# Kernel tuning notes

Measured on AMD Instinct MI355X. Metric: run time of the kernel, lower is better.

Reference implementation:

```python
import jax, jax.numpy as jnp
import numpy as np
from jax import lax

B, L, D = 4, 4096, 1024
EXP = 2
DI = D * EXP
K_PERC = 7
KS_DIFF = 3
DILATIONS = (1, 4, 16)


def _dwconv(h, w, dil):
    # h: [B, C, L] channels-first, w: [C, 1, k] depthwise kernel (groups=C)
    k = w.shape[-1]
    pad = dil * (k // 2)
    return lax.conv_general_dilated(
        h, w, window_strides=(1,), padding=[(pad, pad)],
        rhs_dilation=(dil,), dimension_numbers=("NCH", "OIH", "NCH"),
        feature_group_count=w.shape[0])


def _layernorm(x, g, b, eps=1e-5):
    m = jnp.mean(x, axis=-1, keepdims=True)
    v = jnp.mean(jnp.square(x - m), axis=-1, keepdims=True)
    return (x - m) * lax.rsqrt(v + eps) * g + b


def setup_inputs() -> dict:
    key = jax.random.key(0)
    ks = jax.random.split(key, 16)
    n = lambda k, shape, scale: (jax.random.normal(k, shape, dtype=jnp.float32) * scale)
    inp = {
        "x": n(ks[0], (B, L, D), 1.0),
        # PerceptionFilter: 3 depthwise convs k=7, pointwise 3D->D, LayerNorm
        "pf_w0": n(ks[1], (D, 1, K_PERC), 0.3),
        "pf_w1": n(ks[2], (D, 1, K_PERC), 0.3),
        "pf_w2": n(ks[3], (D, 1, K_PERC), 0.3),
        "pf_pw": n(ks[4], (D, 3 * D), 1.0 / np.sqrt(3 * D)),
        "ln_g": jnp.ones((D,), jnp.float32),
        "ln_b": jnp.zeros((D,), jnp.float32),
        # ReactionGate: wu/wg: 2D->DI, wd: DI->D, alpha
        "rg_wu": n(ks[5], (DI, 2 * D), 1.0 / np.sqrt(2 * D)),
        "rg_wg": n(ks[6], (DI, 2 * D), 1.0 / np.sqrt(2 * D)),
        "rg_wd": n(ks[7], (D, DI), 1.0 / np.sqrt(DI)),
        "rg_alpha": jnp.full((D,), 0.1, jnp.float32),
        # MultiRateDiffusion: 3 depthwise dilated convs k=3, selector D->3, strength
        "md_w0": n(ks[8], (D, 1, KS_DIFF), 0.3),
        "md_w1": n(ks[9], (D, 1, KS_DIFF), 0.3),
        "md_w2": n(ks[10], (D, 1, KS_DIFF), 0.3),
        "md_sel": n(ks[11], (len(DILATIONS), D), 1.0 / np.sqrt(D)),
        "md_strength": jnp.asarray(0.1, jnp.float32),
    }
    return inp


def reference(x, pf_w0, pf_w1, pf_w2, pf_pw, ln_g, ln_b,
              rg_wu, rg_wg, rg_wd, rg_alpha,
              md_w0, md_w1, md_w2, md_sel, md_strength):
    # --- PerceptionFilter ---
    h = jnp.swapaxes(x, 1, 2)  # [B, D, L]
    pcat = jnp.concatenate([_dwconv(h, w, 1) for w in (pf_w0, pf_w1, pf_w2)], axis=1)  # [B, 3D, L]
    p = jnp.einsum("bcl,dc->bld", pcat, pf_pw)  # pointwise 1x1 conv -> [B, L, D]
    p = _layernorm(p, ln_g, ln_b)
    # --- ReactionGate ---
    cat = jnp.concatenate([x, p], axis=-1)  # [B, L, 2D]
    u = cat @ rg_wu.T
    g = jax.nn.sigmoid(cat @ rg_wg.T)
    x2 = x + rg_alpha * ((g * jax.nn.silu(u)) @ rg_wd.T)
    # --- MultiRateDiffusion ---
    h2 = jnp.swapaxes(x2, 1, 2)  # [B, D, L]
    diffs = jnp.stack([_dwconv(h2, w, dil) for w, dil in
                       zip((md_w0, md_w1, md_w2), DILATIONS)], axis=-1)  # [B, D, L, R]
    wsel = jax.nn.softmax(x2 @ md_sel.T, axis=-1)[:, None]  # [B, 1, L, R]
    combined = jnp.swapaxes(jnp.sum(diffs * wsel, axis=-1), 1, 2)  # [B, L, D]
    return x2 + md_strength * (combined - x2)
```

## Files before the change

### kernel.cpp

```cpp
#include <hip/hip_runtime.h>

#define LL 4096
#define BL 16384

typedef __attribute__((ext_vector_type(4))) float f32x4;
typedef __attribute__((ext_vector_type(4))) int i32x4;
typedef __attribute__((ext_vector_type(4))) unsigned short u16x4;
typedef unsigned short ushort_t;
typedef unsigned int u32;

static __device__ __forceinline__ unsigned short f2bf(float f) {
    union { float f; unsigned int i; } v; v.f = f;
    unsigned int r = v.i + 0x7fffu + ((v.i >> 16) & 1u);
    return (unsigned short)(r >> 16);
}
static __device__ __forceinline__ float bf2f(unsigned short u) {
    union { unsigned int i; float f; } v; v.i = ((unsigned int)u) << 16; return v.f;
}
static __device__ __forceinline__ int qclamp(float x, float s) {
    return (int)rintf(fminf(fmaxf(x * s, -127.f), 127.f));
}
static __device__ __forceinline__ int q4(float a, float b, float c, float d, float s) {
    return (qclamp(a,s) & 255) | ((qclamp(b,s) & 255) << 8) |
           ((qclamp(c,s) & 255) << 16) | ((qclamp(d,s) & 255) << 24);
}

static __device__ __forceinline__ i32x4 mfma_i8(i32x4 a, i32x4 b, i32x4 c) {
    asm("v_mfma_i32_16x16x64_i8 %0, %1, %2, %0" : "+v"(c) : "v"(a), "v"(b));
    return c;
}

static __device__ __forceinline__ void gload16(const char* g, char* l) {
    __builtin_amdgcn_global_load_lds(
        (const __attribute__((address_space(1))) u32*)g,
        (__attribute__((address_space(3))) u32*)l, 16, 0, 0);
}

#define BAR()   asm volatile("s_barrier" ::: "memory")
#define VMW0()  asm volatile("s_waitcnt vmcnt(0)" ::: "memory")

__global__ __launch_bounds__(256) void cvt_all(
    const float* __restrict__ wu, const float* __restrict__ wg,
    const float* __restrict__ pw, const float* __restrict__ wd,
    char* __restrict__ wug8, char* __restrict__ wpw8, char* __restrict__ wd8,
    float sW, float sW1)
{
    int blk = blockIdx.x;
    if (blk < 4096) {
        int r = blk;
        int type = (r >> 4) & 1;
        int src = ((r >> 5) << 4) | (r & 15);
        const float* sp = (type ? wg : wu) + (size_t)src * 2048;
        char* d = wug8 + (size_t)r * 2048;
        int i = threadIdx.x;
        f32x4 v0 = ((const f32x4*)sp)[2 * i];
        f32x4 v1 = ((const f32x4*)sp)[2 * i + 1];
        ((int*)d)[2 * i]     = q4(v0[0], v0[1], v0[2], v0[3], sW);
        ((int*)d)[2 * i + 1] = q4(v1[0], v1[1], v1[2], v1[3], sW);
    } else if (blk < 4096 + 3072) {
        int i = (blk - 4096) * 256 + threadIdx.x;
        f32x4 v = ((const f32x4*)pw)[i];
        ((int*)wpw8)[i] = q4(v[0], v[1], v[2], v[3], sW1);
    } else {
        int i = (blk - 4096 - 3072) * 256 + threadIdx.x;
        f32x4 v = ((const f32x4*)wd)[i];
        ((int*)wd8)[i] = q4(v[0], v[1], v[2], v[3], sW);
    }
}

__global__ __launch_bounds__(256) void pf_conv(
    const float* __restrict__ x,
    const float* __restrict__ w0, const float* __restrict__ w1, const float* __restrict__ w2,
    char* __restrict__ pcat, char* __restrict__ cat, float sP, float sX)
{
    int bl = blockIdx.x;
    int b = bl >> 12;
    int l = bl & 4095;
    int c0 = threadIdx.x << 2;

    f32x4 v[7];
#pragma unroll
    for (int t = 0; t < 7; ++t) {
        int ls = l + t - 3;
        if (ls >= 0 && ls < LL)
            v[t] = *(const f32x4*)(x + (((size_t)b * LL + ls) << 10) + c0);
        else {
            f32x4 z = {0.f, 0.f, 0.f, 0.f};
            v[t] = z;
        }
    }
    *(int*)(cat + (((size_t)bl) << 11) + c0) = q4(v[3][0], v[3][1], v[3][2], v[3][3], sX);
    const float* ww[3] = { w0, w1, w2 };
#pragma unroll
    for (int j = 0; j < 3; ++j) {
        const float* w = ww[j];
        float a[4];
#pragma unroll
        for (int e = 0; e < 4; ++e) {
            int c = c0 + e;
            float s = 0.f;
#pragma unroll
            for (int t = 0; t < 7; ++t) s += v[t][e] * w[c * 7 + t];
            a[e] = s;
        }
        *(int*)(pcat + (size_t)bl * 3072 + j * 1024 + c0) = q4(a[0], a[1], a[2], a[3], sP);
    }
}

__global__ __launch_bounds__(256) void ln_kernel(
    const ushort_t* __restrict__ p, const float* __restrict__ g,
    const float* __restrict__ bta, char* __restrict__ cat, float sX)
{
    int bl = blockIdx.x;
    int tid = threadIdx.x;
    int c0 = tid << 2;
    u16x4 pv = *(const u16x4*)(p + (((size_t)bl) << 10) + c0);
    float v0 = bf2f(pv[0]), v1 = bf2f(pv[1]), v2 = bf2f(pv[2]), v3 = bf2f(pv[3]);
    float s  = v0 + v1 + v2 + v3;
    float sq = v0*v0 + v1*v1 + v2*v2 + v3*v3;
#pragma unroll
    for (int off = 32; off > 0; off >>= 1) {
        s  += __shfl_down(s, off);
        sq += __shfl_down(sq, off);
    }
    __shared__ float rs[4], rq[4];
    int w = tid >> 6;
    if ((tid & 63) == 0) { rs[w] = s; rq[w] = sq; }
    __syncthreads();
    float S = rs[0] + rs[1] + rs[2] + rs[3];
    float Q = rq[0] + rq[1] + rq[2] + rq[3];
    float m   = S * (1.f / 1024.f);
    float var = Q * (1.f / 1024.f) - m * m;
    float inv = rsqrtf(var + 1e-5f);
    f32x4 gv = *(const f32x4*)(g + c0);
    f32x4 bv = *(const f32x4*)(bta + c0);
    *(int*)(cat + (((size_t)bl) << 11) + 1024 + c0) =
        q4((v0-m)*inv*gv[0]+bv[0], (v1-m)*inv*gv[1]+bv[1],
           (v2-m)*inv*gv[2]+bv[2], (v3-m)*inv*gv[3]+bv[3], sX);
}

template<int MODE>
__global__ __launch_bounds__(512, 2) void gemm8i(
    const char* __restrict__ A, const char* __restrict__ Bm,
    ushort_t* __restrict__ C16, char* __restrict__ C8,
    const float* __restrict__ X, const float* __restrict__ alpha,
    int N, int K, int lgny, float invS, float sOut)
{
    __shared__ char smem[131072];
    const int tid = threadIdx.x;
    const int wid = tid >> 6, lane = tid & 63;
    const int fr = lane & 15, fq = lane >> 4;
    const int wm = (wid >> 2) * 128;
    const int wn = (wid & 3) * 64;

    const int nwg = gridDim.x * gridDim.y;
    const int orig = blockIdx.y * gridDim.x + blockIdx.x;
    const int q = nwg >> 3;
    const int tile = (orig & 7) * q + (orig >> 3);
    const int m0 = (tile >> lgny) * 256;
    const int n0 = (tile & ((1 << lgny) - 1)) * 256;

    const int srow = tid >> 3;
    const int gch = ((tid & 7) ^ (srow & 7)) * 16;

    const char* gp[8];
    int lpo[8];
#pragma unroll
    for (int op = 0; op < 2; ++op)
#pragma unroll
        for (int j = 0; j < 4; ++j) {
            int idx = op * 4 + j;
            const char* gs = op ? Bm : A;
            int rb = op ? n0 : m0;
            gp[idx] = gs + (size_t)(rb + j * 64 + srow) * K + gch;
            lpo[idx] = op * 32768 + (j * 64 + srow) * 128 + (tid & 7) * 16;
        }

    const int ach0 = ((fq) ^ (fr & 7)) * 16;
    const int ach1 = ((4 + fq) ^ (fr & 7)) * 16;
    const int arow = (wm + fr) * 128;
    const int brow = 32768 + (wn + fr) * 128;

    i32x4 acc[8][4] = {};
    const int NT = K >> 7;

#define STAGE_ALL(koff, d) do {                                             \
    _Pragma("unroll") for (int i_ = 0; i_ < 8; ++i_)                        \
        gload16(gp[i_] + (koff), smem + (d) * 65536 + lpo[i_]);             \
    } while (0)

    STAGE_ALL(0, 0);
    VMW0();
    BAR();

    for (int t = 0; t < NT; ++t) {
        const int c = t & 1;
        const bool st = (t + 1 < NT);
        const char* base = smem + c * 65536;

        if (st) STAGE_ALL((size_t)(t + 1) * 128, c ^ 1);

        i32x4 b0[4], b1[4], a0[4], a1[4];
#pragma unroll
        for (int n_ = 0; n_ < 4; ++n_) {
            b0[n_] = *(const i32x4*)(base + brow + n_ * 2048 + ach0);
            b1[n_] = *(const i32x4*)(base + brow + n_ * 2048 + ach1);
        }
#pragma unroll
        for (int i_ = 0; i_ < 4; ++i_) {
            a0[i_] = *(const i32x4*)(base + arow + i_ * 2048 + ach0);
            a1[i_] = *(const i32x4*)(base + arow + i_ * 2048 + ach1);
        }
        __builtin_amdgcn_s_setprio(1);
#pragma unroll
        for (int i_ = 0; i_ < 4; ++i_)
#pragma unroll
            for (int n_ = 0; n_ < 4; ++n_) {
                acc[i_][n_] = mfma_i8(a0[i_], b0[n_], acc[i_][n_]);
                acc[i_][n_] = mfma_i8(a1[i_], b1[n_], acc[i_][n_]);
            }
        __builtin_amdgcn_s_setprio(0);
#pragma unroll
        for (int i_ = 0; i_ < 4; ++i_) {
            a0[i_] = *(const i32x4*)(base + arow + (4 + i_) * 2048 + ach0);
            a1[i_] = *(const i32x4*)(base + arow + (4 + i_) * 2048 + ach1);
        }
        __builtin_amdgcn_s_setprio(1);
#pragma unroll
        for (int i_ = 0; i_ < 4; ++i_)
#pragma unroll
            for (int n_ = 0; n_ < 4; ++n_) {
                acc[4 + i_][n_] = mfma_i8(a0[i_], b0[n_], acc[4 + i_][n_]);
                acc[4 + i_][n_] = mfma_i8(a1[i_], b1[n_], acc[4 + i_][n_]);
            }
        __builtin_amdgcn_s_setprio(0);

        if (st) VMW0();
        BAR();
    }
#undef STAGE_ALL

    const int mbase = m0 + wm + fq * 4;
#pragma unroll
    for (int mi = 0; mi < 8; ++mi) {
        if (MODE == 1) {
#pragma unroll
            for (int pi = 0; pi < 2; ++pi)
#pragma unroll
                for (int r = 0; r < 4; ++r) {
                    float u = (float)acc[mi][2 * pi][r] * invS;
                    float g = (float)acc[mi][2 * pi + 1][r] * invS;
                    float sg = 1.f / (1.f + __expf(-g));
                    float sl = u / (1.f + __expf(-u));
                    int col = ((n0 + wn) >> 1) + pi * 16 + fr;
                    C8[(size_t)(mbase + mi * 16 + r) * (N >> 1) + col] =
                        (char)qclamp(sg * sl, sOut);
                }
        } else {
#pragma unroll
            for (int ni = 0; ni < 4; ++ni)
#pragma unroll
                for (int r = 0; r < 4; ++r) {
                    int row = mbase + mi * 16 + r;
                    int col = n0 + wn + ni * 16 + fr;
                    size_t idx = (size_t)row * N + col;
                    float vv = (float)acc[mi][ni][r] * invS;
                    if (MODE == 0) C16[idx] = f2bf(vv);
                    else           C16[idx] = f2bf(X[idx] + alpha[col] * vv);
                }
        }
    }
}

__global__ __launch_bounds__(256) void diffusion(
    const ushort_t* __restrict__ x2,
    const float* __restrict__ w0, const float* __restrict__ w1, const float* __restrict__ w2,
    const float* __restrict__ sel, const float* __restrict__ strength_p,
    float* __restrict__ out)
{
    int bl = blockIdx.x;
    int b = bl >> 12;
    int l = bl & 4095;
    int tid = threadIdx.x;
    int c0 = tid << 2;
    const ushort_t* base = x2 + (((size_t)b * LL) << 10);

    u16x4 xcv = *(const u16x4*)(x2 + (((size_t)bl) << 10) + c0);
    float xc0 = bf2f(xcv[0]), xc1 = bf2f(xcv[1]), xc2 = bf2f(xcv[2]), xc3 = bf2f(xcv[3]);
    f32x4 s0 = *(const f32x4*)(sel + c0);
    f32x4 s1 = *(const f32x4*)(sel + 1024 + c0);
    f32x4 s2 = *(const f32x4*)(sel + 2048 + c0);
    float t0 = xc0*s0[0] + xc1*s0[1] + xc2*s0[2] + xc3*s0[3];
    float t1 = xc0*s1[0] + xc1*s1[1] + xc2*s1[2] + xc3*s1[3];
    float t2 = xc0*s2[0] + xc1*s2[1] + xc2*s2[2] + xc3*s2[3];
#pragma unroll
    for (int off = 32; off > 0; off >>= 1) {
        t0 += __shfl_down(t0, off);
        t1 += __shfl_down(t1, off);
        t2 += __shfl_down(t2, off);
    }
    __shared__ float r0[4], r1[4], r2[4];
    int w = tid >> 6;
    if ((tid & 63) == 0) { r0[w] = t0; r1[w] = t1; r2[w] = t2; }
    __syncthreads();
    float L0 = r0[0] + r0[1] + r0[2] + r0[3];
    float L1 = r1[0] + r1[1] + r1[2] + r1[3];
    float L2 = r2[0] + r2[1] + r2[2] + r2[3];
    float mx = fmaxf(L0, fmaxf(L1, L2));
    float e0 = __expf(L0 - mx), e1 = __expf(L1 - mx), e2 = __expf(L2 - mx);
    float inv = 1.f / (e0 + e1 + e2);
    float ws0 = e0 * inv, ws1 = e1 * inv, ws2 = e2 * inv;
    float stg = *strength_p;

    float comb0 = 0.f, comb1 = 0.f, comb2 = 0.f, comb3 = 0.f;
    const float* wset[3] = { w0, w1, w2 };
    const int dils[3] = { 1, 4, 16 };
    const float wsel[3] = { ws0, ws1, ws2 };
#pragma unroll
    for (int r = 0; r < 3; ++r) {
        const float* wp = wset[r] + (size_t)c0 * 3;
        float wf[12];
        *(f32x4*)&wf[0] = *(const f32x4*)(wp + 0);
        *(f32x4*)&wf[4] = *(const f32x4*)(wp + 4);
        *(f32x4*)&wf[8] = *(const f32x4*)(wp + 8);
        int dil = dils[r];
        float d0 = 0.f, d1 = 0.f, d2 = 0.f, d3 = 0.f;
#pragma unroll
        for (int t = 0; t < 3; ++t) {
            int ls = l + (t - 1) * dil;
            float xv0 = 0.f, xv1 = 0.f, xv2 = 0.f, xv3 = 0.f;
            if (ls >= 0 && ls < LL) {
                u16x4 xv = *(const u16x4*)(base + (((size_t)ls) << 10) + c0);
                xv0 = bf2f(xv[0]); xv1 = bf2f(xv[1]); xv2 = bf2f(xv[2]); xv3 = bf2f(xv[3]);
            }
            d0 += xv0 * wf[0 * 3 + t];
            d1 += xv1 * wf[1 * 3 + t];
            d2 += xv2 * wf[2 * 3 + t];
            d3 += xv3 * wf[3 * 3 + t];
        }
        comb0 += wsel[r] * d0; comb1 += wsel[r] * d1;
        comb2 += wsel[r] * d2; comb3 += wsel[r] * d3;
    }
    f32x4 o = { xc0 + stg * (comb0 - xc0), xc1 + stg * (comb1 - xc1),
                xc2 + stg * (comb2 - xc2), xc3 + stg * (comb3 - xc3) };
    *(f32x4*)(out + (((size_t)bl) << 10) + c0) = o;
}

extern "C" void kernel_launch(void* const* d_in, const int* in_sizes, int n_in,
                              void* d_out, int out_size, void* d_ws, size_t ws_size,
                              hipStream_t stream)
{
    const float* x      = (const float*)d_in[0];
    const float* pf_w0  = (const float*)d_in[1];
    const float* pf_w1  = (const float*)d_in[2];
    const float* pf_w2  = (const float*)d_in[3];
    const float* pf_pw  = (const float*)d_in[4];
    const float* ln_g   = (const float*)d_in[5];
    const float* ln_b   = (const float*)d_in[6];
    const float* rg_wu  = (const float*)d_in[7];
    const float* rg_wg  = (const float*)d_in[8];
    const float* rg_wd  = (const float*)d_in[9];
    const float* rg_al  = (const float*)d_in[10];
    const float* md_w0  = (const float*)d_in[11];
    const float* md_w1  = (const float*)d_in[12];
    const float* md_w2  = (const float*)d_in[13];
    const float* md_sel = (const float*)d_in[14];
    const float* md_str = (const float*)d_in[15];
    float* outp = (float*)d_out;

    const float sP  = 127.f / 5.f;
    const float sX  = 127.f / 6.f;
    const float sW1 = 127.f / 0.11f;
    const float sW  = 127.f / 0.14f;
    const float invS1 = 1.f / (sP * sW1);
    const float invS2 = 1.f / (sX * sW);

    char* ws = (char*)d_ws;
    size_t off = 0;
    char*     pcat8 = (char*)   (ws + off); off += (size_t)BL * 3072;
    char*     cat8  = (char*)   (ws + off); off += (size_t)BL * 2048;
    ushort_t* ppre  = (ushort_t*)(ws + off); off += (size_t)BL * 1024 * 2;
    char*     wpw8  = (char*)   (ws + off); off += (size_t)1024 * 3072;
    char*     wug8  = (char*)   (ws + off); off += (size_t)4096 * 2048;
    char*     wd8   = (char*)   (ws + off); off += (size_t)1024 * 2048;
    char*     act8  = pcat8;
    ushort_t* x2    = ppre;

    cvt_all<<<4096 + 3072 + 2048, 256, 0, stream>>>(
        rg_wu, rg_wg, pf_pw, rg_wd, wug8, wpw8, wd8, sW, sW1);

    pf_conv<<<BL, 256, 0, stream>>>(x, pf_w0, pf_w1, pf_w2, pcat8, cat8, sP, sX);

    gemm8i<0><<<dim3(64, 4), 512, 0, stream>>>(
        pcat8, wpw8, ppre, nullptr, nullptr, nullptr, 1024, 3072, 2, invS1, 0.f);

    ln_kernel<<<BL, 256, 0, stream>>>(ppre, ln_g, ln_b, cat8, sX);

    gemm8i<1><<<dim3(64, 16), 512, 0, stream>>>(
        cat8, wug8, nullptr, act8, nullptr, nullptr, 4096, 2048, 4, invS2, sX);

    gemm8i<2><<<dim3(64, 4), 512, 0, stream>>>(
        act8, wd8, x2, nullptr, x, rg_al, 1024, 2048, 2, invS2, 0.f);

    diffusion<<<BL, 256, 0, stream>>>(x2, md_w0, md_w1, md_w2, md_sel, md_str, outp);
}
```

Baseline: 451.2 us.

## Switch int8 GEMM to 32x32x32 MFMA tiles with reworked fragment loads

Replaces the 16x16x64 int8 MFMA with the 32x32x32 variant, so each wave computes 4x2 blocks of 32x32 accumulators instead of 8x4 blocks of 16x16. LDS fragment addressing and swizzle are recomputed for the new lane mapping. The epilogues are rewritten, with the gated MODE 1 path using a lane shuffle to pair u and g columns. The aim is fewer LDS fragment reads per MFMA. The trade-off is a more complex epilogue, half-idle lanes in the gated store, and possible correctness risk in the interleaved u/g column mapping.

Result: slower. 537.2 us (+19.1%).

```diff
diff --git a/kernel.cpp b/kernel.cpp
--- a/kernel.cpp
+++ b/kernel.cpp
@@ -5,6 +5,7 @@
 
 typedef __attribute__((ext_vector_type(4))) float f32x4;
 typedef __attribute__((ext_vector_type(4))) int i32x4;
+typedef __attribute__((ext_vector_type(16))) int i32x16;
 typedef __attribute__((ext_vector_type(4))) unsigned short u16x4;
 typedef unsigned short ushort_t;
 typedef unsigned int u32;
@@ -25,8 +26,8 @@
            ((qclamp(c,s) & 255) << 16) | ((qclamp(d,s) & 255) << 24);
 }
 
-static __device__ __forceinline__ i32x4 mfma_i8(i32x4 a, i32x4 b, i32x4 c) {
-    asm("v_mfma_i32_16x16x64_i8 %0, %1, %2, %0" : "+v"(c) : "v"(a), "v"(b));
+static __device__ __forceinline__ i32x16 mfma_i8_32(i32x4 a, i32x4 b, i32x16 c) {
+    asm("v_mfma_i32_32x32x32_i8 %0, %1, %2, %0" : "+v"(c) : "v"(a), "v"(b));
     return c;
 }
 
@@ -149,7 +150,7 @@
     __shared__ char smem[131072];
     const int tid = threadIdx.x;
     const int wid = tid >> 6, lane = tid & 63;
-    const int fr = lane & 15, fq = lane >> 4;
+    const int l31 = lane & 31, hi = lane >> 5, l7 = lane & 7;
     const int wm = (wid >> 2) * 128;
     const int wn = (wid & 3) * 64;
 
@@ -176,12 +177,13 @@
             lpo[idx] = op * 32768 + (j * 64 + srow) * 128 + (tid & 7) * 16;
         }
 
-    const int ach0 = ((fq) ^ (fr & 7)) * 16;
-    const int ach1 = ((4 + fq) ^ (fr & 7)) * 16;
-    const int arow = (wm + fr) * 128;
-    const int brow = 32768 + (wn + fr) * 128;
-
-    i32x4 acc[8][4] = {};
+    int chk[4];
+#pragma unroll
+    for (int ks = 0; ks < 4; ++ks) chk[ks] = ((ks * 2 + hi) ^ l7) * 16;
+    const int arow = (wm + l31) * 128;
+    const int brow = 32768 + (wn + l31) * 128;
+
+    i32x16 acc[4][2] = {};
     const int NT = K >> 7;
 
 #define STAGE_ALL(koff, d) do {                                             \
@@ -200,76 +202,66 @@
 
         if (st) STAGE_ALL((size_t)(t + 1) * 128, c ^ 1);
 
-        i32x4 b0[4], b1[4], a0[4], a1[4];
-#pragma unroll
-        for (int n_ = 0; n_ < 4; ++n_) {
-            b0[n_] = *(const i32x4*)(base + brow + n_ * 2048 + ach0);
-            b1[n_] = *(const i32x4*)(base + brow + n_ * 2048 + ach1);
-        }
-#pragma unroll
-        for (int i_ = 0; i_ < 4; ++i_) {
-            a0[i_] = *(const i32x4*)(base + arow + i_ * 2048 + ach0);
-            a1[i_] = *(const i32x4*)(base + arow + i_ * 2048 + ach1);
-        }
-        __builtin_amdgcn_s_setprio(1);
-#pragma unroll
-        for (int i_ = 0; i_ < 4; ++i_)
-#pragma unroll
-            for (int n_ = 0; n_ < 4; ++n_) {
-                acc[i_][n_] = mfma_i8(a0[i_], b0[n_], acc[i_][n_]);
-                acc[i_][n_] = mfma_i8(a1[i_], b1[n_], acc[i_][n_]);
-            }
-        __builtin_amdgcn_s_setprio(0);
-#pragma unroll
-        for (int i_ = 0; i_ < 4; ++i_) {
-            a0[i_] = *(const i32x4*)(base + arow + (4 + i_) * 2048 + ach0);
-            a1[i_] = *(const i32x4*)(base + arow + (4 + i_) * 2048 + ach1);
-        }
-        __builtin_amdgcn_s_setprio(1);
-#pragma unroll
-        for (int i_ = 0; i_ < 4; ++i_)
-#pragma unroll
-            for (int n_ = 0; n_ < 4; ++n_) {
-                acc[4 + i_][n_] = mfma_i8(a0[i_], b0[n_], acc[4 + i_][n_]);
-                acc[4 + i_][n_] = mfma_i8(a1[i_], b1[n_], acc[4 + i_][n_]);
-            }
-        __builtin_amdgcn_s_setprio(0);
+#pragma unroll
+        for (int h = 0; h < 2; ++h) {
+            i32x4 b[2][2], a[4][2];
+#pragma unroll
+            for (int ti = 0; ti < 2; ++ti)
+#pragma unroll
+                for (int s_ = 0; s_ < 2; ++s_)
+                    b[ti][s_] = *(const i32x4*)(base + brow + ti * 4096 + chk[2 * h + s_]);
+#pragma unroll
+            for (int mi = 0; mi < 4; ++mi)
+#pragma unroll
+                for (int s_ = 0; s_ < 2; ++s_)
+                    a[mi][s_] = *(const i32x4*)(base + arow + mi * 4096 + chk[2 * h + s_]);
+            __builtin_amdgcn_s_setprio(1);
+#pragma unroll
+            for (int mi = 0; mi < 4; ++mi)
+#pragma unroll
+                for (int ti = 0; ti < 2; ++ti)
+#pragma unroll
+                    for (int s_ = 0; s_ < 2; ++s_)
+                        acc[mi][ti] = mfma_i8_32(a[mi][s_], b[ti][s_], acc[mi][ti]);
+            __builtin_amdgcn_s_setprio(0);
+        }
 
         if (st) VMW0();
         BAR();
     }
 #undef STAGE_ALL
 
-    const int mbase = m0 + wm + fq * 4;
-#pragma unroll
-    for (int mi = 0; mi < 8; ++mi) {
-        if (MODE == 1) {
-#pragma unroll
-            for (int pi = 0; pi < 2; ++pi)
-#pragma unroll
-                for (int r = 0; r < 4; ++r) {
-                    float u = (float)acc[mi][2 * pi][r] * invS;
-                    float g = (float)acc[mi][2 * pi + 1][r] * invS;
+#pragma unroll
+    for (int mi = 0; mi < 4; ++mi)
+#pragma unroll
+        for (int ti = 0; ti < 2; ++ti) {
+            if (MODE == 1) {
+                int colb = ((n0 + wn + ti * 32) >> 1) + (lane & 15);
+#pragma unroll
+                for (int r = 0; r < 16; ++r) {
+                    int val = acc[mi][ti][r];
+                    int pv = __shfl_xor(val, 16);
+                    float u = (float)((lane & 16) ? pv : val) * invS;
+                    float g = (float)((lane & 16) ? val : pv) * invS;
                     float sg = 1.f / (1.f + __expf(-g));
                     float sl = u / (1.f + __expf(-u));
-                    int col = ((n0 + wn) >> 1) + pi * 16 + fr;
-                    C8[(size_t)(mbase + mi * 16 + r) * (N >> 1) + col] =
-                        (char)qclamp(sg * sl, sOut);
+                    if (!(lane & 16)) {
+                        int row = m0 + wm + mi * 32 + (r & 3) + 8 * (r >> 2) + 4 * hi;
+                        C8[(size_t)row * (N >> 1) + colb] = (char)qclamp(sg * sl, sOut);
+                    }
                 }
-        } else {
-#pragma unroll
-            for (int ni = 0; ni < 4; ++ni)
-#pragma unroll
-                for (int r = 0; r < 4; ++r) {
-                    int row = mbase + mi * 16 + r;
-                    int col = n0 + wn + ni * 16 + fr;
+            } else {
+                int col = n0 + wn + ti * 32 + l31;
+#pragma unroll
+                for (int r = 0; r < 16; ++r) {
+                    int row = m0 + wm + mi * 32 + (r & 3) + 8 * (r >> 2) + 4 * hi;
                     size_t idx = (size_t)row * N + col;
-                    float vv = (float)acc[mi][ni][r] * invS;
+                    float vv = (float)acc[mi][ti][r] * invS;
                     if (MODE == 0) C16[idx] = f2bf(vv);
                     else           C16[idx] = f2bf(X[idx] + alpha[col] * vv);
                 }
-        }
-    }
+            }
+        }
 }
 
 __global__ __launch_bounds__(256) void diffusion(
```
